# Kernel optimization log

Measured on AMD Instinct MI355X. Metric: run time of the kernel, lower is better.

The kernel has to match this reference:

```python
import jax, jax.numpy as jnp
import numpy as np

B, S, HID, HEADS = 2, 2048, 256, 8
HD = HID // HEADS
SCALE = float(np.sqrt(HD))  # torch: math.sqrt(hid_dim // n_heads)


def setup_inputs() -> dict:
    key = jax.random.key(0)
    ks = jax.random.split(key, 13)
    lim = 1.0 / np.sqrt(HID)  # nn.Linear default init range
    def lin(k):
        k1, k2 = jax.random.split(k)
        W = jax.random.uniform(k1, (HID, HID), jnp.float32, -lim, lim)
        b = jax.random.uniform(k2, (HID,), jnp.float32, -lim, lim)
        return W, b
    Wq, bq = lin(ks[0]); Wk, bk = lin(ks[1]); Wv, bv = lin(ks[2]); Wfc, bfc = lin(ks[3])
    return {
        "query": jax.random.normal(ks[4], (B, S, HID), jnp.float32),
        "key": jax.random.normal(ks[5], (B, S, HID), jnp.float32),
        "value": jax.random.normal(ks[6], (B, S, HID), jnp.float32),
        "compound_pos": jax.random.normal(ks[7], (B, HEADS, S, S), jnp.float32) * 0.02,
        "mask": jax.random.randint(ks[8], (B, 1, 1, S), 0, 2, jnp.int32),
        "Wq": Wq, "bq": bq, "Wk": Wk, "bk": bk, "Wv": Wv, "bv": bv,
        "Wfc": Wfc, "bfc": bfc,
    }


def reference(query, key, value, compound_pos, mask, Wq, bq, Wk, bk, Wv, bv, Wfc, bfc):
    bsz, s, _ = query.shape
    # QKV projections, split heads: [B,S,HID] -> [B,H,S,HD]
    Q = (query @ Wq.T + bq).reshape(bsz, s, HEADS, HD).transpose(0, 2, 1, 3)
    K = (key @ Wk.T + bk).reshape(bsz, -1, HEADS, HD).transpose(0, 2, 1, 3)
    V = (value @ Wv.T + bv).reshape(bsz, -1, HEADS, HD).transpose(0, 2, 1, 3)
    energy = jnp.einsum("bhqd,bhkd->bhqk", Q, K) / SCALE + compound_pos
    energy = jnp.where(mask == 0, -jnp.inf, energy)
    attn = jax.nn.softmax(energy, axis=-1)  # dropout is identity in eval mode
    x = jnp.einsum("bhqk,bhkd->bhqd", attn, V)
    x = x.transpose(0, 2, 1, 3).reshape(bsz, s, HID)
    return x @ Wfc.T + bfc
```

## Files before the change

kernel.cpp:

```cpp
#include <hip/hip_runtime.h>
#include <hip/hip_bf16.h>

#define HIDDIM 256
#define NHEADS 8
#define HEADDIM 32
#define SEQ 2048
#define NBATCH 2
#define NTOK (NBATCH * SEQ)
#define RSCALE 0.17677669529663687f
#define LOG2E 1.4426950408889634f
#define NSEG 2
#define SEGLEN (SEQ / NSEG)
#define CHUNK 64
#define NCH (SEGLEN / CHUNK)

typedef __attribute__((ext_vector_type(8))) short bfrag;
typedef __attribute__((ext_vector_type(4))) float f32x4;
typedef __attribute__((ext_vector_type(8))) float f32x8;
typedef __attribute__((ext_vector_type(2))) unsigned u32x2;

static __device__ __forceinline__ short f2bs(float x) {
    __hip_bfloat16 h = __float2bfloat16(x);
    return *reinterpret_cast<short*>(&h);
}
static __device__ __forceinline__ unsigned pack2(float a, float b) {
    return (unsigned(f2bs(a)) & 0xffffu) | (unsigned(f2bs(b)) << 16);
}
static __device__ __forceinline__ void gll16(const void* g, void* l) {
    __builtin_amdgcn_global_load_lds(
        (const __attribute__((address_space(1))) void*)g,
        (__attribute__((address_space(3))) void*)l, 16, 0, 0);
}

__global__ __launch_bounds__(256) void prep_kernel(
    const float* __restrict__ Wq, const float* __restrict__ Wk,
    const float* __restrict__ Wv, const float* __restrict__ Wfc,
    short* __restrict__ Whi)
{
    const int idx = blockIdx.x * 256 + threadIdx.x;
    const int w = blockIdx.y;
    const float* src = (w == 0) ? Wq : (w == 1) ? Wk : (w == 2) ? Wv : Wfc;
    Whi[w * 65536 + idx] = f2bs(src[idx]);
}

__global__ __launch_bounds__(256) void maskbits_kernel(
    const int* __restrict__ mask, unsigned* __restrict__ mb)
{
    const int i = blockIdx.x * 256 + threadIdx.x;
    const unsigned long long bal = __ballot(mask[i] != 0);
    if ((threadIdx.x & 63) == 0) {
        const int w = i >> 5;
        mb[w]     = (unsigned)bal;
        mb[w + 1] = (unsigned)(bal >> 32);
    }
}

__global__ __launch_bounds__(256) void qkv_kernel(
    const float* __restrict__ qin, const float* __restrict__ kin,
    const float* __restrict__ vin,
    const float* __restrict__ bq, const float* __restrict__ bk,
    const float* __restrict__ bv,
    const short* __restrict__ Whi,
    short* __restrict__ Qw, short* __restrict__ Kw, short* __restrict__ Vt)
{
    const int lane = threadIdx.x & 63;
    const int wid  = threadIdx.x >> 6;
    const int lr = lane & 15, lg = lane >> 4;
    const int which = blockIdx.z;

    const float* in   = which == 0 ? qin : (which == 1 ? kin : vin);
    const float* bias = which == 0 ? bq  : (which == 1 ? bk  : bv);
    const short* W = Whi + which * 65536;

    const int row0 = blockIdx.x * 64 + wid * 16;
    const int col0 = blockIdx.y * 128;

    f32x4 acc[8] = {};
    const float* arow = in + (size_t)(row0 + lr) * HIDDIM + lg * 8;
    #pragma unroll
    for (int k0 = 0; k0 < HIDDIM; k0 += 32) {
        const f32x8 af = *(const f32x8*)(arow + k0);
        bfrag a;
        #pragma unroll
        for (int j = 0; j < 8; ++j) a[j] = f2bs(af[j]);
        #pragma unroll
        for (int nt = 0; nt < 8; ++nt) {
            const bfrag bf = *(const bfrag*)(W + (size_t)(col0 + nt * 16 + lr) * HIDDIM + k0 + lg * 8);
            acc[nt] = __builtin_amdgcn_mfma_f32_16x16x32_bf16(a, bf, acc[nt], 0, 0, 0);
        }
    }

    #pragma unroll
    for (int nt = 0; nt < 8; ++nt) {
        const int col = col0 + nt * 16 + lr;
        const float bval = bias[col];
        #pragma unroll
        for (int r = 0; r < 4; ++r) {
            const int row = row0 + lg * 4 + r;
            float v = acc[nt][r] + bval;
            if (which == 0) {
                Qw[(size_t)row * HIDDIM + col] = f2bs(v * (RSCALE * LOG2E));
            } else if (which == 1) {
                Kw[(size_t)row * HIDDIM + col] = f2bs(v);
            } else {
                const int h = col >> 5, d = col & 31;
                const int bb = row >> 11, ss = row & (SEQ - 1);
                Vt[(((size_t)(bb * NHEADS + h) * HEADDIM + d) << 11) + ss] = f2bs(v);
            }
        }
    }
}

__global__ __launch_bounds__(256, 4) void attn_kernel(
    const short* __restrict__ Q, const short* __restrict__ K,
    const short* __restrict__ Vt,
    const float* __restrict__ pos,
    const unsigned* __restrict__ mbits,
    float* __restrict__ Op, float* __restrict__ Sp)
{
    const int lane = threadIdx.x & 63;
    const int wid  = threadIdx.x >> 6;
    const int lr = lane & 15, lg = lane >> 4;

    const int lb = blockIdx.x + 32 * (blockIdx.y + 16 * blockIdx.z);
    const int work = ((lb & 7) << 7) | (lb >> 3);
    const int xb = work & 31;
    const int bh = (work >> 5) & 15;
    const int zb = work >> 9;
    const int b = bh >> 3, h = bh & 7;
    const int phase = work & 15;

    const int qblk = xb * 4 + wid;
    const int q0 = qblk * 16;
    const int c0 = zb * SEGLEN;

    __shared__ short KVb[3][8][512];
    __shared__ short Pl[4][16][68];

    unsigned mw[32];
    {
        const unsigned* mwp = mbits + b * 64 + (c0 >> 5);
        #pragma unroll
        for (int j = 0; j < 32; ++j)
            mw[j] = __builtin_amdgcn_readfirstlane(mwp[(j + 2 * phase) & 31]);
    }

    const bfrag qf = *(const bfrag*)(Q + (size_t)(b * SEQ + q0 + lr) * HIDDIM + h * HEADDIM + lg * 8);

    const short* Kg = K + (size_t)b * SEQ * HIDDIM + h * HEADDIM + lg * 8;
    const int vtile = wid >> 1, vsub = wid & 1;
    const short* Vg = Vt + ((size_t)(bh * HEADDIM + vtile * 16 + lr) << 11) + vsub * 32 + lg * 8;

    const float* posb = pos + (size_t)(bh * SEQ + q0 + lr) * SEQ;

    f32x4 posr[3][4];
    f32x4 o0 = {}, o1 = {};
    float s_acc = 0.0f;

    {
        const int ca = c0 + phase * CHUNK;
        const int cb2 = c0 + (((1 + phase) & 15) * CHUNK);
        gll16(Kg + (size_t)(ca + wid * 16 + lr) * HIDDIM, &KVb[0][wid][lane * 8]);
        gll16(Vg + ca, &KVb[0][4 + wid][lane * 8]);
        __builtin_amdgcn_sched_barrier(0);
        #pragma unroll
        for (int tt = 0; tt < 4; ++tt)
            posr[0][tt] = *(const f32x4*)(posb + ca + tt * 16 + lg * 4);
        __builtin_amdgcn_sched_barrier(0);
        gll16(Kg + (size_t)(cb2 + wid * 16 + lr) * HIDDIM, &KVb[1][wid][lane * 8]);
        gll16(Vg + cb2, &KVb[1][4 + wid][lane * 8]);
        __builtin_amdgcn_sched_barrier(0);
        #pragma unroll
        for (int tt = 0; tt < 4; ++tt)
            posr[1][tt] = *(const f32x4*)(posb + cb2 + tt * 16 + lg * 4);
        __builtin_amdgcn_sched_barrier(0);
    }

    #pragma unroll
    for (int t = 0; t < NCH; ++t) {
        const int cur = t % 3;
        const int c = c0 + (((t + phase) & 15) * CHUNK);

        if (t < NCH - 1) { asm volatile("s_waitcnt vmcnt(6)" ::: "memory"); }
        else             { asm volatile("s_waitcnt vmcnt(0)" ::: "memory"); }
        __builtin_amdgcn_sched_barrier(0);
        __builtin_amdgcn_s_barrier();
        __builtin_amdgcn_sched_barrier(0);

        if (t + 2 < NCH) {
            const int cn = c0 + (((t + 2 + phase) & 15) * CHUNK);
            gll16(Kg + (size_t)(cn + wid * 16 + lr) * HIDDIM, &KVb[(t + 2) % 3][wid][lane * 8]);
            gll16(Vg + cn, &KVb[(t + 2) % 3][4 + wid][lane * 8]);
        }
        __builtin_amdgcn_sched_barrier(0);

        f32x4 e[4];
        #pragma unroll
        for (int tt = 0; tt < 4; ++tt) {
            const bfrag kf = *(const bfrag*)&KVb[cur][tt][lane * 8];
            const f32x4 z = {};
            e[tt] = __builtin_amdgcn_mfma_f32_16x16x32_bf16(kf, qf, z, 0, 0, 0);
        }

        if (t + 2 < NCH) {
            const int cn = c0 + (((t + 2 + phase) & 15) * CHUNK);
            #pragma unroll
            for (int tt = 0; tt < 4; ++tt)
                posr[(t + 2) % 3][tt] = *(const f32x4*)(posb + cn + tt * 16 + lg * 4);
        }
        __builtin_amdgcn_sched_barrier(0);

        #pragma unroll
        for (int tt = 0; tt < 4; ++tt) {
            const unsigned shifted = mw[t * 2 + (tt >> 1)] >> (((tt & 1) << 4) + (lg << 2));
            float p[4];
            #pragma unroll
            for (int r = 0; r < 4; ++r) {
                const float ev = exp2f(fmaf(posr[cur][tt][r], LOG2E, e[tt][r]));
                p[r] = (shifted & (1u << r)) ? ev : 0.0f;
                s_acc += p[r];
            }
            u32x2 w = { pack2(p[0], p[1]), pack2(p[2], p[3]) };
            *(u32x2*)&Pl[wid][lr][tt * 16 + lg * 4] = w;
        }

        #pragma unroll
        for (int s = 0; s < 2; ++s) {
            const bfrag pf  = *(const bfrag*)&Pl[wid][lr][s * 32 + lg * 8];
            const bfrag vf0 = *(const bfrag*)&KVb[cur][4 + 0 + s][lane * 8];
            const bfrag vf1 = *(const bfrag*)&KVb[cur][4 + 2 + s][lane * 8];
            o0 = __builtin_amdgcn_mfma_f32_16x16x32_bf16(vf0, pf, o0, 0, 0, 0);
            o1 = __builtin_amdgcn_mfma_f32_16x16x32_bf16(vf1, pf, o1, 0, 0, 0);
        }
    }

    s_acc += __shfl_xor(s_acc, 16, 64);
    s_acc += __shfl_xor(s_acc, 32, 64);

    float* Ow = Op + (((size_t)(zb * 16 + bh) * 128 + qblk) * 512) + lr * 32;
    *(f32x4*)(Ow + lg * 4)      = o0;
    *(f32x4*)(Ow + 16 + lg * 4) = o1;
    if (lg == 0)
        Sp[((size_t)(zb * 16 + bh) * 128 + qblk) * 16 + lr] = s_acc;
}

__global__ __launch_bounds__(256) void combine_kernel(
    const float* __restrict__ Op, const float* __restrict__ Sp,
    short* __restrict__ X)
{
    const int lane = threadIdx.x & 63;
    const int wid  = threadIdx.x >> 6;
    const int lr = lane & 15, lg = lane >> 4;
    const int idx = blockIdx.x * 4 + wid;
    const int bh = idx >> 7, qblk = idx & 127;
    const int b = bh >> 3, h = bh & 7, q0 = qblk * 16;

    __shared__ short Xt[4][16][40];

    f32x4 o0 = {}, o1 = {};
    float s = 0.0f;
    #pragma unroll
    for (int sz = 0; sz < NSEG; ++sz) {
        const float* Ow = Op + (((size_t)(sz * 16 + bh) * 128 + qblk) * 512) + lr * 32;
        o0 += *(const f32x4*)(Ow + lg * 4);
        o1 += *(const f32x4*)(Ow + 16 + lg * 4);
        s  += Sp[((size_t)(sz * 16 + bh) * 128 + qblk) * 16 + lr];
    }
    const float inv = 1.0f / s;

    u32x2 w0 = { pack2(o0[0] * inv, o0[1] * inv), pack2(o0[2] * inv, o0[3] * inv) };
    u32x2 w1 = { pack2(o1[0] * inv, o1[1] * inv), pack2(o1[2] * inv, o1[3] * inv) };
    *(u32x2*)&Xt[wid][lr][lg * 4]      = w0;
    *(u32x2*)&Xt[wid][lr][16 + lg * 4] = w1;

    const bfrag xr = *(const bfrag*)&Xt[wid][lr][lg * 8];
    *(bfrag*)(X + (size_t)(b * SEQ + q0 + lr) * HIDDIM + h * HEADDIM + lg * 8) = xr;
}

__global__ __launch_bounds__(256) void fc_kernel(
    const short* __restrict__ X,
    const short* __restrict__ Whi,
    const float* __restrict__ bias,
    float* __restrict__ out)
{
    const int lane = threadIdx.x & 63;
    const int wid  = threadIdx.x >> 6;
    const int lr = lane & 15, lg = lane >> 4;

    const int row0 = blockIdx.x * 64 + wid * 16;
    const int col0 = blockIdx.y * 64;
    const short* W = Whi + 3 * 65536;

    f32x4 acc[4] = {};
    const short* arow = X + (size_t)(row0 + lr) * HIDDIM + lg * 8;
    #pragma unroll
    for (int k0 = 0; k0 < HIDDIM; k0 += 32) {
        const bfrag a = *(const bfrag*)(arow + k0);
        #pragma unroll
        for (int nt = 0; nt < 4; ++nt) {
            const bfrag bf = *(const bfrag*)(W + (size_t)(col0 + nt * 16 + lr) * HIDDIM + k0 + lg * 8);
            acc[nt] = __builtin_amdgcn_mfma_f32_16x16x32_bf16(a, bf, acc[nt], 0, 0, 0);
        }
    }

    #pragma unroll
    for (int nt = 0; nt < 4; ++nt) {
        const int col = col0 + nt * 16 + lr;
        const float bval = bias[col];
        #pragma unroll
        for (int r = 0; r < 4; ++r) {
            const int row = row0 + lg * 4 + r;
            out[(size_t)row * HIDDIM + col] = acc[nt][r] + bval;
        }
    }
}

extern "C" void kernel_launch(void* const* d_in, const int* in_sizes, int n_in,
                              void* d_out, int out_size, void* d_ws, size_t ws_size,
                              hipStream_t stream)
{
    (void)in_sizes; (void)n_in; (void)out_size; (void)ws_size;

    const float* qin  = (const float*)d_in[0];
    const float* kin  = (const float*)d_in[1];
    const float* vin  = (const float*)d_in[2];
    const float* pos  = (const float*)d_in[3];
    const int*   mask = (const int*)d_in[4];
    const float* Wq   = (const float*)d_in[5];
    const float* bq   = (const float*)d_in[6];
    const float* Wk   = (const float*)d_in[7];
    const float* bk   = (const float*)d_in[8];
    const float* Wv   = (const float*)d_in[9];
    const float* bv   = (const float*)d_in[10];
    const float* Wfc  = (const float*)d_in[11];
    const float* bfc  = (const float*)d_in[12];
    float* out = (float*)d_out;

    short* ws  = (short*)d_ws;
    short* Whi = ws;
    short* Qw  = Whi + 4 * 65536;
    short* Kw  = Qw + (size_t)NTOK * HIDDIM;
    short* Vt  = Kw + (size_t)NTOK * HIDDIM;
    short* Xws = Vt + (size_t)NTOK * HIDDIM;
    float* Op  = (float*)(Xws + (size_t)NTOK * HIDDIM);
    float* Sp  = Op + (size_t)NSEG * 16 * 128 * 512;
    unsigned* Mb = (unsigned*)(Sp + (size_t)NSEG * 16 * 128 * 16);

    prep_kernel<<<dim3(65536 / 256, 4), 256, 0, stream>>>(Wq, Wk, Wv, Wfc, Whi);
    maskbits_kernel<<<dim3(NTOK / 256), 256, 0, stream>>>(mask, Mb);
    qkv_kernel<<<dim3(NTOK / 64, 2, 3), 256, 0, stream>>>(
        qin, kin, vin, bq, bk, bv, Whi, Qw, Kw, Vt);
    attn_kernel<<<dim3(SEQ / 64, NBATCH * NHEADS, NSEG), 256, 0, stream>>>(
        Qw, Kw, Vt, pos, Mb, Op, Sp);
    combine_kernel<<<dim3(NBATCH * NHEADS * 128 / 4), 256, 0, stream>>>(Op, Sp, Xws);
    fc_kernel<<<dim3(NTOK / 64, HIDDIM / 64), 256, 0, stream>>>(
        Xws, Whi, bfc, out);
}
```

Measured before the change: 102.9 us.

## Drop key-split in attention, fuse combine into attention, merge maskbits into prep

Removes the two-segment split over keys, so each attention block processes the full sequence and normalizes and writes bf16 X directly. This eliminates the combine kernel and the fp32 partial-output round trip. The separate maskbits kernel is folded into the weight-prep kernel, and mask bits are repacked per lane into nibbles held in registers. The trade-off is half as many attention blocks (512 instead of 1024), with occupancy hint lowered to 2, which may leave CUs underfilled and expose latency on the dominant pos stream.

```diff
diff --git a/kernel.cpp b/kernel.cpp
--- a/kernel.cpp
+++ b/kernel.cpp
@@ -9,10 +9,8 @@
 #define NTOK (NBATCH * SEQ)
 #define RSCALE 0.17677669529663687f
 #define LOG2E 1.4426950408889634f
-#define NSEG 2
-#define SEGLEN (SEQ / NSEG)
 #define CHUNK 64
-#define NCH (SEGLEN / CHUNK)
+#define NCH (SEQ / CHUNK)
 
 typedef __attribute__((ext_vector_type(8))) short bfrag;
 typedef __attribute__((ext_vector_type(4))) float f32x4;
@@ -35,23 +33,20 @@
 __global__ __launch_bounds__(256) void prep_kernel(
     const float* __restrict__ Wq, const float* __restrict__ Wk,
     const float* __restrict__ Wv, const float* __restrict__ Wfc,
-    short* __restrict__ Whi)
+    const int* __restrict__ mask,
+    short* __restrict__ Whi, unsigned* __restrict__ mb)
 {
     const int idx = blockIdx.x * 256 + threadIdx.x;
     const int w = blockIdx.y;
     const float* src = (w == 0) ? Wq : (w == 1) ? Wk : (w == 2) ? Wv : Wfc;
     Whi[w * 65536 + idx] = f2bs(src[idx]);
-}
-
-__global__ __launch_bounds__(256) void maskbits_kernel(
-    const int* __restrict__ mask, unsigned* __restrict__ mb)
-{
-    const int i = blockIdx.x * 256 + threadIdx.x;
-    const unsigned long long bal = __ballot(mask[i] != 0);
-    if ((threadIdx.x & 63) == 0) {
-        const int w = i >> 5;
-        mb[w]     = (unsigned)bal;
-        mb[w + 1] = (unsigned)(bal >> 32);
+    if (w == 0 && idx < NTOK) {
+        const unsigned long long bal = __ballot(mask[idx] != 0);
+        if ((threadIdx.x & 63) == 0) {
+            const int wd = idx >> 5;
+            mb[wd]     = (unsigned)bal;
+            mb[wd + 1] = (unsigned)(bal >> 32);
+        }
     }
 }
 
@@ -111,38 +106,50 @@
     }
 }
 
-__global__ __launch_bounds__(256, 4) void attn_kernel(
+__global__ __launch_bounds__(256, 2) void attn_kernel(
     const short* __restrict__ Q, const short* __restrict__ K,
     const short* __restrict__ Vt,
     const float* __restrict__ pos,
     const unsigned* __restrict__ mbits,
-    float* __restrict__ Op, float* __restrict__ Sp)
+    short* __restrict__ X)
 {
     const int lane = threadIdx.x & 63;
     const int wid  = threadIdx.x >> 6;
     const int lr = lane & 15, lg = lane >> 4;
 
-    const int lb = blockIdx.x + 32 * (blockIdx.y + 16 * blockIdx.z);
-    const int work = ((lb & 7) << 7) | (lb >> 3);
+    const int lb = blockIdx.x + 32 * blockIdx.y;
+    const int work = ((lb & 7) << 6) | (lb >> 3);
     const int xb = work & 31;
-    const int bh = (work >> 5) & 15;
-    const int zb = work >> 9;
+    const int bh = work >> 5;
     const int b = bh >> 3, h = bh & 7;
-    const int phase = work & 15;
+    const int phase = work & 31;
 
     const int qblk = xb * 4 + wid;
     const int q0 = qblk * 16;
-    const int c0 = zb * SEGLEN;
 
     __shared__ short KVb[3][8][512];
     __shared__ short Pl[4][16][68];
-
-    unsigned mw[32];
+    __shared__ short Xt[4][16][40];
+
+    unsigned mvk[16];
     {
-        const unsigned* mwp = mbits + b * 64 + (c0 >> 5);
-        #pragma unroll
-        for (int j = 0; j < 32; ++j)
-            mw[j] = __builtin_amdgcn_readfirstlane(mwp[(j + 2 * phase) & 31]);
+        const unsigned* mwp = mbits + b * 64;
+        const int sh = lg << 2;
+        #pragma unroll
+        for (int j = 0; j < 32; j += 2) {
+            unsigned half[2];
+            #pragma unroll
+            for (int u = 0; u < 2; ++u) {
+                const int a = (j + u + phase) & 31;
+                const u32x2 wp = *(const u32x2*)(mwp + 2 * a);
+                const unsigned w0 = wp[0], w1 = wp[1];
+                half[u] = ((w0 >> sh) & 0xFu)
+                        | (((w0 >> (16 + sh)) & 0xFu) << 4)
+                        | (((w1 >> sh) & 0xFu) << 8)
+                        | (((w1 >> (16 + sh)) & 0xFu) << 12);
+            }
+            mvk[j >> 1] = half[0] | (half[1] << 16);
+        }
     }
 
     const bfrag qf = *(const bfrag*)(Q + (size_t)(b * SEQ + q0 + lr) * HIDDIM + h * HEADDIM + lg * 8);
@@ -158,8 +165,8 @@
     float s_acc = 0.0f;
 
     {
-        const int ca = c0 + phase * CHUNK;
-        const int cb2 = c0 + (((1 + phase) & 15) * CHUNK);
+        const int ca  = (phase & 31) * CHUNK;
+        const int cb2 = ((1 + phase) & 31) * CHUNK;
         gll16(Kg + (size_t)(ca + wid * 16 + lr) * HIDDIM, &KVb[0][wid][lane * 8]);
         gll16(Vg + ca, &KVb[0][4 + wid][lane * 8]);
         __builtin_amdgcn_sched_barrier(0);
@@ -179,7 +186,7 @@
     #pragma unroll
     for (int t = 0; t < NCH; ++t) {
         const int cur = t % 3;
-        const int c = c0 + (((t + phase) & 15) * CHUNK);
+        const int c = ((t + phase) & 31) * CHUNK;
 
         if (t < NCH - 1) { asm volatile("s_waitcnt vmcnt(6)" ::: "memory"); }
         else             { asm volatile("s_waitcnt vmcnt(0)" ::: "memory"); }
@@ -188,7 +195,7 @@
         __builtin_amdgcn_sched_barrier(0);
 
         if (t + 2 < NCH) {
-            const int cn = c0 + (((t + 2 + phase) & 15) * CHUNK);
+            const int cn = ((t + 2 + phase) & 31) * CHUNK;
             gll16(Kg + (size_t)(cn + wid * 16 + lr) * HIDDIM, &KVb[(t + 2) % 3][wid][lane * 8]);
             gll16(Vg + cn, &KVb[(t + 2) % 3][4 + wid][lane * 8]);
         }
@@ -203,7 +210,7 @@
         }
 
         if (t + 2 < NCH) {
-            const int cn = c0 + (((t + 2 + phase) & 15) * CHUNK);
+            const int cn = ((t + 2 + phase) & 31) * CHUNK;
             #pragma unroll
             for (int tt = 0; tt < 4; ++tt)
                 posr[(t + 2) % 3][tt] = *(const f32x4*)(posb + cn + tt * 16 + lg * 4);
@@ -212,12 +219,12 @@
 
         #pragma unroll
         for (int tt = 0; tt < 4; ++tt) {
-            const unsigned shifted = mw[t * 2 + (tt >> 1)] >> (((tt & 1) << 4) + (lg << 2));
+            const unsigned nib = mvk[t >> 1] >> (((t & 1) << 4) + (tt << 2));
             float p[4];
             #pragma unroll
             for (int r = 0; r < 4; ++r) {
                 const float ev = exp2f(fmaf(posr[cur][tt][r], LOG2E, e[tt][r]));
-                p[r] = (shifted & (1u << r)) ? ev : 0.0f;
+                p[r] = (nib & (1u << r)) ? ev : 0.0f;
                 s_acc += p[r];
             }
             u32x2 w = { pack2(p[0], p[1]), pack2(p[2], p[3]) };
@@ -236,45 +243,16 @@
 
     s_acc += __shfl_xor(s_acc, 16, 64);
     s_acc += __shfl_xor(s_acc, 32, 64);
-
-    float* Ow = Op + (((size_t)(zb * 16 + bh) * 128 + qblk) * 512) + lr * 32;
-    *(f32x4*)(Ow + lg * 4)      = o0;
-    *(f32x4*)(Ow + 16 + lg * 4) = o1;
-    if (lg == 0)
-        Sp[((size_t)(zb * 16 + bh) * 128 + qblk) * 16 + lr] = s_acc;
-}
-
-__global__ __launch_bounds__(256) void combine_kernel(
-    const float* __restrict__ Op, const float* __restrict__ Sp,
-    short* __restrict__ X)
-{
-    const int lane = threadIdx.x & 63;
-    const int wid  = threadIdx.x >> 6;
-    const int lr = lane & 15, lg = lane >> 4;
-    const int idx = blockIdx.x * 4 + wid;
-    const int bh = idx >> 7, qblk = idx & 127;
-    const int b = bh >> 3, h = bh & 7, q0 = qblk * 16;
-
-    __shared__ short Xt[4][16][40];
-
-    f32x4 o0 = {}, o1 = {};
-    float s = 0.0f;
-    #pragma unroll
-    for (int sz = 0; sz < NSEG; ++sz) {
-        const float* Ow = Op + (((size_t)(sz * 16 + bh) * 128 + qblk) * 512) + lr * 32;
-        o0 += *(const f32x4*)(Ow + lg * 4);
-        o1 += *(const f32x4*)(Ow + 16 + lg * 4);
-        s  += Sp[((size_t)(sz * 16 + bh) * 128 + qblk) * 16 + lr];
-    }
-    const float inv = 1.0f / s;
-
-    u32x2 w0 = { pack2(o0[0] * inv, o0[1] * inv), pack2(o0[2] * inv, o0[3] * inv) };
-    u32x2 w1 = { pack2(o1[0] * inv, o1[1] * inv), pack2(o1[2] * inv, o1[3] * inv) };
-    *(u32x2*)&Xt[wid][lr][lg * 4]      = w0;
-    *(u32x2*)&Xt[wid][lr][16 + lg * 4] = w1;
-
-    const bfrag xr = *(const bfrag*)&Xt[wid][lr][lg * 8];
-    *(bfrag*)(X + (size_t)(b * SEQ + q0 + lr) * HIDDIM + h * HEADDIM + lg * 8) = xr;
+    const float inv = 1.0f / s_acc;
+
+    {
+        u32x2 w0 = { pack2(o0[0] * inv, o0[1] * inv), pack2(o0[2] * inv, o0[3] * inv) };
+        u32x2 w1 = { pack2(o1[0] * inv, o1[1] * inv), pack2(o1[2] * inv, o1[3] * inv) };
+        *(u32x2*)&Xt[wid][lr][lg * 4]      = w0;
+        *(u32x2*)&Xt[wid][lr][16 + lg * 4] = w1;
+        const bfrag xr = *(const bfrag*)&Xt[wid][lr][lg * 8];
+        *(bfrag*)(X + (size_t)(b * SEQ + q0 + lr) * HIDDIM + h * HEADDIM + lg * 8) = xr;
+    }
 }
 
 __global__ __launch_bounds__(256) void fc_kernel(
@@ -342,17 +320,13 @@
     short* Kw  = Qw + (size_t)NTOK * HIDDIM;
     short* Vt  = Kw + (size_t)NTOK * HIDDIM;
     short* Xws = Vt + (size_t)NTOK * HIDDIM;
-    float* Op  = (float*)(Xws + (size_t)NTOK * HIDDIM);
-    float* Sp  = Op + (size_t)NSEG * 16 * 128 * 512;
-    unsigned* Mb = (unsigned*)(Sp + (size_t)NSEG * 16 * 128 * 16);
-
-    prep_kernel<<<dim3(65536 / 256, 4), 256, 0, stream>>>(Wq, Wk, Wv, Wfc, Whi);
-    maskbits_kernel<<<dim3(NTOK / 256), 256, 0, stream>>>(mask, Mb);
+    unsigned* Mb = (unsigned*)(Xws + (size_t)NTOK * HIDDIM);
+
+    prep_kernel<<<dim3(65536 / 256, 4), 256, 0, stream>>>(Wq, Wk, Wv, Wfc, mask, Whi, Mb);
     qkv_kernel<<<dim3(NTOK / 64, 2, 3), 256, 0, stream>>>(
         qin, kin, vin, bq, bk, bv, Whi, Qw, Kw, Vt);
-    attn_kernel<<<dim3(SEQ / 64, NBATCH * NHEADS, NSEG), 256, 0, stream>>>(
-        Qw, Kw, Vt, pos, Mb, Op, Sp);
-    combine_kernel<<<dim3(NBATCH * NHEADS * 128 / 4), 256, 0, stream>>>(Op, Sp, Xws);
+    attn_kernel<<<dim3(SEQ / 64, NBATCH * NHEADS), 256, 0, stream>>>(
+        Qw, Kw, Vt, pos, Mb, Xws);
     fc_kernel<<<dim3(NTOK / 64, HIDDIM / 64), 256, 0, stream>>>(
         Xws, Whi, bfc, out);
 }
```

New measurement: 284.1 us. +176.1%, slower.
